# Kernel optimization log

Measured on AMD Instinct MI355X. Metric: run time of the kernel, lower is better.

## Reference

```python
import jax, jax.numpy as jnp
import numpy as np

D_IN = 1024
D_OUT = 1024
SEQ = 4096


def setup_inputs() -> dict:
    key = jax.random.key(0)
    kx, kq, kk, kv = jax.random.split(key, 4)
    x = jax.random.normal(kx, (SEQ, D_IN), dtype=jnp.float32)
    # original uses torch.rand (uniform [0,1)) for parameter init
    w_query = jax.random.uniform(kq, (D_IN, D_OUT), dtype=jnp.float32)
    w_key = jax.random.uniform(kk, (D_IN, D_OUT), dtype=jnp.float32)
    w_value = jax.random.uniform(kv, (D_IN, D_OUT), dtype=jnp.float32)
    return {"x": x, "w_query": w_query, "w_key": w_key, "w_value": w_value}


def reference(x, w_query, w_key, w_value):
    # QKV projections: [S, d_in] @ [d_in, d_out] -> [S, d_out]
    queries = x @ w_query
    keys = x @ w_key
    values = x @ w_value
    scale = keys.shape[-1] ** 0.5
    # full attention matrix [S, S]
    attn_scores = jnp.einsum('sd,td->st', queries, keys)
    attn_weights = jax.nn.softmax(attn_scores / scale, axis=-1)
    context_vecs = attn_weights @ values  # [S, d_out]
    return context_vecs
```

## Files before the change

### kernel.cpp

```cpp
#include <hip/hip_runtime.h>
#include <hip/hip_fp16.h>
#include <math.h>

#define SEQ    4096
#define DMODEL 1024

typedef _Float16 half8   __attribute__((ext_vector_type(8)));
typedef _Float16 half4v  __attribute__((ext_vector_type(4)));
typedef float    floatx4 __attribute__((ext_vector_type(4)));

__device__ inline void split_val(float v, _Float16& h, _Float16& l) {
    _Float16 hh = (_Float16)v;
    h = hh;
    l = (_Float16)(v - (float)hh);
}

__global__ __launch_bounds__(256) void prep(const float* __restrict__ x,
                                            const float* __restrict__ wq,
                                            const float* __restrict__ wk,
                                            const float* __restrict__ wv,
                                            _Float16* __restrict__ x_hi,
                                            _Float16* __restrict__ x_lo,
                                            _Float16* __restrict__ wqkT_hi,
                                            _Float16* __restrict__ wqkT_lo,
                                            _Float16* __restrict__ wvT) {
    __shared__ float tile[32][33];
    const int b = blockIdx.x;
    if (b < 3072) {
        const int which = b >> 10;
        const int bb = b & 1023;
        const int c0 = (bb & 31) * 32;
        const int r0 = (bb >> 5) * 32;
        const float* w = (which == 0) ? wq : (which == 1) ? wk : wv;
        const int tx = threadIdx.x & 31, ty = threadIdx.x >> 5;
#pragma unroll
        for (int j = 0; j < 4; ++j)
            tile[ty * 4 + j][tx] = w[(size_t)(r0 + ty * 4 + j) * DMODEL + c0 + tx];
        __syncthreads();
        if (which < 2) {
            _Float16* th = wqkT_hi + (size_t)which * DMODEL * DMODEL;
            _Float16* tl = wqkT_lo + (size_t)which * DMODEL * DMODEL;
#pragma unroll
            for (int j = 0; j < 4; ++j) {
                float v = tile[tx][ty * 4 + j];
                size_t idx = (size_t)(c0 + ty * 4 + j) * DMODEL + r0 + tx;
                _Float16 h, l;
                split_val(v, h, l);
                th[idx] = h;
                tl[idx] = l;
            }
        } else {
#pragma unroll
            for (int j = 0; j < 4; ++j)
                wvT[(size_t)(c0 + ty * 4 + j) * DMODEL + r0 + tx] =
                    (_Float16)tile[tx][ty * 4 + j];
        }
    } else {
        const int t0 = (b - 3072) * 256 + threadIdx.x;
#pragma unroll
        for (int rep = 0; rep < 4; ++rep) {
            const size_t i = (size_t)t0 + (size_t)rep * 262144;
            floatx4 v = *(const floatx4*)(x + 4 * i);
            half4v h, l;
#pragma unroll
            for (int j = 0; j < 4; ++j) {
                _Float16 hh = (_Float16)v[j];
                _Float16 ll = (_Float16)(v[j] - (float)hh);
                h[j] = hh;
                l[j] = ll;
            }
            *(half4v*)(x_hi + 4 * i) = h;
            *(half4v*)(x_lo + 4 * i) = l;
        }
    }
}

__global__ __launch_bounds__(512, 1) void gemm_qkproj_dp(
    const _Float16* __restrict__ Ahi, const _Float16* __restrict__ Alo,
    const _Float16* __restrict__ Bhi, const _Float16* __restrict__ Blo,
    _Float16* __restrict__ Qcat, _Float16* __restrict__ Kcat) {
    __shared__ _Float16 As[4][128][32];
    __shared__ _Float16 Bs[4][256][32];

    const int tid  = threadIdx.x;
    const int lane = tid & 63;
    const int wid  = tid >> 6;
    const int wm   = (wid >> 2) * 64;
    const int wn   = (wid & 3) * 64;

    const int lin = blockIdx.y * 8 + blockIdx.x;
    const int swz = (lin & 7) * 32 + (lin >> 3);
    const int rowA0 = (swz >> 3) * 128;
    const int colB0 = (swz & 7) * 256;

    const int ar  = tid >> 2;
    const int ag  = tid & 3;
    const int ags = ag ^ ((ar >> 1) & 3);
    const char* aHiB = (const char*)(Ahi + (size_t)(rowA0 + ar) * DMODEL) + ags * 16;
    const char* aLoB = (const char*)(Alo + (size_t)(rowA0 + ar) * DMODEL) + ags * 16;
    const int br  = tid >> 2;
    const int bg  = tid & 3;
    const int bgs = bg ^ ((br >> 1) & 3);
    const char* bHi0 = (const char*)(Bhi + (size_t)(colB0 + br) * DMODEL) + bgs * 16;
    const char* bHi1 = (const char*)(Bhi + (size_t)(colB0 + br + 128) * DMODEL) + bgs * 16;
    const char* bLo0 = (const char*)(Blo + (size_t)(colB0 + br) * DMODEL) + bgs * 16;
    const char* bLo1 = (const char*)(Blo + (size_t)(colB0 + br + 128) * DMODEL) + bgs * 16;

#define STAGE_QA(tt)                                                                 \
    do {                                                                             \
        const int _s = (tt) & 3;                                                     \
        const char* _ab = ((tt) < 64) ? aHiB : aLoB;                                 \
        const size_t _ko = (size_t)((tt) & 31) * 64;                                 \
        __builtin_amdgcn_global_load_lds(                                            \
            (const __attribute__((address_space(1))) void*)(_ab + _ko),              \
            (__attribute__((address_space(3))) void*)&As[_s][ar][ag * 8], 16, 0, 0); \
    } while (0)

#define STAGE_QB(tt)                                                                 \
    do {                                                                             \
        const int _s = (tt) & 3;                                                     \
        const bool _lo = ((tt) >= 32) && ((tt) < 64);                                \
        const char* _b0 = _lo ? bLo0 : bHi0;                                         \
        const char* _b1 = _lo ? bLo1 : bHi1;                                         \
        const size_t _ko = (size_t)((tt) & 31) * 64;                                 \
        __builtin_amdgcn_global_load_lds(                                            \
            (const __attribute__((address_space(1))) void*)(_b0 + _ko),              \
            (__attribute__((address_space(3))) void*)&Bs[_s][br][bg * 8], 16, 0, 0); \
        __builtin_amdgcn_global_load_lds(                                            \
            (const __attribute__((address_space(1))) void*)(_b1 + _ko),              \
            (__attribute__((address_space(3))) void*)&Bs[_s][br + 128][bg * 8], 16, 0, 0);\
    } while (0)

    const int fm = lane & 15;
    const int fq = lane >> 4;
    const int ck = (fq ^ ((fm >> 1) & 3)) * 8;

    floatx4 acc[4][4] = {};

    auto tile_body = [&](int t, bool do_stage) {
        const int s = t & 3;
        half8 av[4], bv01[2];
#pragma unroll
        for (int i = 0; i < 4; ++i) av[i] = *(const half8*)&As[s][wm + i * 16 + fm][ck];
#pragma unroll
        for (int j = 0; j < 2; ++j) bv01[j] = *(const half8*)&Bs[s][wn + j * 16 + fm][ck];
        if (do_stage) STAGE_QA(t + 3);
        asm volatile("" ::: "memory");
        __builtin_amdgcn_s_barrier();
        asm volatile("" ::: "memory");
        __builtin_amdgcn_s_setprio(1);
#pragma unroll
        for (int i = 0; i < 4; ++i)
#pragma unroll
            for (int j = 0; j < 2; ++j)
                acc[i][j] = __builtin_amdgcn_mfma_f32_16x16x32_f16(av[i], bv01[j], acc[i][j], 0, 0, 0);
        __builtin_amdgcn_s_setprio(0);
        asm volatile("" ::: "memory");
        __builtin_amdgcn_s_barrier();
        asm volatile("" ::: "memory");
        half8 bv23[2];
#pragma unroll
        for (int j = 0; j < 2; ++j) bv23[j] = *(const half8*)&Bs[s][wn + 32 + j * 16 + fm][ck];
        if (do_stage) STAGE_QB(t + 3);
        asm volatile("" ::: "memory");
        __builtin_amdgcn_s_barrier();
        asm volatile("" ::: "memory");
        __builtin_amdgcn_s_setprio(1);
#pragma unroll
        for (int i = 0; i < 4; ++i)
#pragma unroll
            for (int j = 0; j < 2; ++j)
                acc[i][j + 2] = __builtin_amdgcn_mfma_f32_16x16x32_f16(av[i], bv23[j], acc[i][j + 2], 0, 0, 0);
        __builtin_amdgcn_s_setprio(0);
    };

    STAGE_QA(0); STAGE_QB(0);
    STAGE_QA(1); STAGE_QB(1);
    STAGE_QA(2); STAGE_QB(2);
    asm volatile("s_waitcnt vmcnt(6)" ::: "memory");
    __builtin_amdgcn_s_barrier();
    asm volatile("" ::: "memory");

#pragma unroll 1
    for (int t = 0; t < 93; ++t) {
        tile_body(t, true);
        asm volatile("s_waitcnt vmcnt(6)" ::: "memory");
        __builtin_amdgcn_s_barrier();
        asm volatile("" ::: "memory");
    }
    tile_body(93, false);
    asm volatile("s_waitcnt vmcnt(3)" ::: "memory");
    __builtin_amdgcn_s_barrier();
    asm volatile("" ::: "memory");
    tile_body(94, false);
    asm volatile("s_waitcnt vmcnt(0)" ::: "memory");
    __builtin_amdgcn_s_barrier();
    asm volatile("" ::: "memory");
    tile_body(95, false);
#undef STAGE_QA
#undef STAGE_QB

    _Float16* dcat = Qcat;
    int cbase = colB0;
    if (colB0 >= 1024) { dcat = Kcat; cbase = colB0 - 1024; }

#pragma unroll
    for (int i = 0; i < 4; ++i) {
        const int growb = rowA0 + wm + i * 16 + fq * 4;
#pragma unroll
        for (int j = 0; j < 4; ++j) {
            const int gcol = wn + j * 16 + fm;
#pragma unroll
            for (int r = 0; r < 4; ++r) {
                float v = acc[i][j][r];
                size_t idx = (size_t)(growb + r) * 2048 + cbase + gcol;
                _Float16 h, l;
                split_val(v, h, l);
                dcat[idx] = h;
                dcat[idx + 1024] = l;
            }
        }
    }
}

__global__ __launch_bounds__(512, 2) void gemm_score_dp(
    const _Float16* __restrict__ Qc,
    const _Float16* __restrict__ Kc,
    _Float16* __restrict__ Ph, float* __restrict__ Marr, float* __restrict__ Larr,
    float scale) {
    __shared__ _Float16 As[4][256][32];
    __shared__ _Float16 Bs[4][256][32];

    const int tid  = threadIdx.x;
    const int lane = tid & 63;
    const int wid  = tid >> 6;
    const int wm   = (wid >> 2) * 128;
    const int wn   = (wid & 3) * 64;

    const int lin = blockIdx.y * 16 + blockIdx.x;
    const int swz = (lin & 7) * 32 + (lin >> 3);
    const int rowA0 = (swz >> 4) * 256;
    const int colB0 = (swz & 15) * 256;

    const int pr  = tid >> 2;
    const int pg  = tid & 3;
    const int pgs = pg ^ ((pr >> 1) & 3);

    const char* aSrc0 = (const char*)(Qc + (size_t)(rowA0 + pr) * 2048) + pgs * 16;
    const char* aSrc1 = (const char*)(Qc + (size_t)(rowA0 + pr + 128) * 2048) + pgs * 16;
    const char* bSrc0 = (const char*)(Kc + (size_t)(colB0 + pr) * 2048) + pgs * 16;
    const char* bSrc1 = (const char*)(Kc + (size_t)(colB0 + pr + 128) * 2048) + pgs * 16;

#define STAGE_A(t)                                                                  \
    do {                                                                            \
        const int _s = (t) & 3;                                                     \
        const size_t _ko = (size_t)(t) * 64;                                        \
        __builtin_amdgcn_global_load_lds(                                           \
            (const __attribute__((address_space(1))) void*)(aSrc0 + _ko),           \
            (__attribute__((address_space(3))) void*)&As[_s][pr][pg * 8], 16, 0, 0);\
        __builtin_amdgcn_global_load_lds(                                           \
            (const __attribute__((address_space(1))) void*)(aSrc1 + _ko),           \
            (__attribute__((address_space(3))) void*)&As[_s][pr + 128][pg * 8], 16, 0, 0);\
    } while (0)

#define STAGE_B(t)                                                                  \
    do {                                                                            \
        const int _s = (t) & 3;                                                     \
        const size_t _ko = (size_t)(t) * 64;                                        \
        __builtin_amdgcn_global_load_lds(                                           \
            (const __attribute__((address_space(1))) void*)(bSrc0 + _ko),           \
            (__attribute__((address_space(3))) void*)&Bs[_s][pr][pg * 8], 16, 0, 0);\
        __builtin_amdgcn_global_load_lds(                                           \
            (const __attribute__((address_space(1))) void*)(bSrc1 + _ko),           \
            (__attribute__((address_space(3))) void*)&Bs[_s][pr + 128][pg * 8], 16, 0, 0);\
    } while (0)

    const int fm = lane & 15;
    const int fq = lane >> 4;
    const int ck = (fq ^ ((fm >> 1) & 3)) * 8;

    floatx4 acc[8][4] = {};

    auto tile_body = [&](int t, bool do_stage) {
        const int s = t & 3;
        half8 av[4], bv[4];
#pragma unroll
        for (int i = 0; i < 4; ++i) av[i] = *(const half8*)&As[s][wm + i * 16 + fm][ck];
#pragma unroll
        for (int j = 0; j < 4; ++j) bv[j] = *(const half8*)&Bs[s][wn + j * 16 + fm][ck];
        if (do_stage) STAGE_A(t + 3);
        asm volatile("" ::: "memory");
        __builtin_amdgcn_s_barrier();
        asm volatile("" ::: "memory");
        __builtin_amdgcn_s_setprio(1);
#pragma unroll
        for (int i = 0; i < 4; ++i)
#pragma unroll
            for (int j = 0; j < 4; ++j)
                acc[i][j] = __builtin_amdgcn_mfma_f32_16x16x32_f16(av[i], bv[j], acc[i][j], 0, 0, 0);
        __builtin_amdgcn_s_setprio(0);
        asm volatile("" ::: "memory");
        __builtin_amdgcn_s_barrier();
        asm volatile("" ::: "memory");
        half8 av2[4];
#pragma unroll
        for (int i = 0; i < 4; ++i) av2[i] = *(const half8*)&As[s][wm + 64 + i * 16 + fm][ck];
        if (do_stage) STAGE_B(t + 3);
        asm volatile("" ::: "memory");
        __builtin_amdgcn_s_barrier();
        asm volatile("" ::: "memory");
        __builtin_amdgcn_s_setprio(1);
#pragma unroll
        for (int i = 0; i < 4; ++i)
#pragma unroll
            for (int j = 0; j < 4; ++j)
                acc[i + 4][j] = __builtin_amdgcn_mfma_f32_16x16x32_f16(av2[i], bv[j], acc[i + 4][j], 0, 0, 0);
        __builtin_amdgcn_s_setprio(0);
    };

    STAGE_A(0); STAGE_B(0);
    STAGE_A(1); STAGE_B(1);
    STAGE_A(2); STAGE_B(2);
    asm volatile("s_waitcnt vmcnt(8)" ::: "memory");
    __builtin_amdgcn_s_barrier();
    asm volatile("" ::: "memory");

#pragma unroll 1
    for (int t = 0; t < 61; ++t) {
        tile_body(t, true);
        asm volatile("s_waitcnt vmcnt(8)" ::: "memory");
        __builtin_amdgcn_s_barrier();
        asm volatile("" ::: "memory");
    }
    tile_body(61, false);
    asm volatile("s_waitcnt vmcnt(4)" ::: "memory");
    __builtin_amdgcn_s_barrier();
    asm volatile("" ::: "memory");
    tile_body(62, false);
    asm volatile("s_waitcnt vmcnt(0)" ::: "memory");
    __builtin_amdgcn_s_barrier();
    asm volatile("" ::: "memory");
    tile_body(63, false);
#undef STAGE_A
#undef STAGE_B

    const int tprime = (colB0 + wn) >> 6;
#pragma unroll
    for (int i = 0; i < 8; ++i) {
#pragma unroll
        for (int r = 0; r < 4; ++r) {
            const int grow = rowA0 + wm + i * 16 + fq * 4 + r;
            float s0 = acc[i][0][r] * scale;
            float s1 = acc[i][1][r] * scale;
            float s2 = acc[i][2][r] * scale;
            float s3 = acc[i][3][r] * scale;
            float mx = fmaxf(fmaxf(s0, s1), fmaxf(s2, s3));
            mx = fmaxf(mx, __shfl_xor(mx, 1));
            mx = fmaxf(mx, __shfl_xor(mx, 2));
            mx = fmaxf(mx, __shfl_xor(mx, 4));
            mx = fmaxf(mx, __shfl_xor(mx, 8));
            float p0 = __expf(s0 - mx);
            float p1 = __expf(s1 - mx);
            float p2 = __expf(s2 - mx);
            float p3 = __expf(s3 - mx);
            float sum = p0 + p1 + p2 + p3;
            sum += __shfl_xor(sum, 1);
            sum += __shfl_xor(sum, 2);
            sum += __shfl_xor(sum, 4);
            sum += __shfl_xor(sum, 8);
            _Float16* prow = Ph + (size_t)grow * SEQ + colB0 + wn + fm;
            prow[0]  = (_Float16)p0;
            prow[16] = (_Float16)p1;
            prow[32] = (_Float16)p2;
            prow[48] = (_Float16)p3;
            if (fm == 0) {
                Marr[(size_t)grow * 64 + tprime] = mx;
                Larr[(size_t)grow * 64 + tprime] = sum;
            }
        }
    }
}

__global__ __launch_bounds__(256) void reduce_scale(const float* __restrict__ Marr,
                                                    const float* __restrict__ Larr,
                                                    _Float16* __restrict__ P) {
    __shared__ float c_tab[64];
    const int tid = threadIdx.x;
    const int row = blockIdx.x;

    if (tid < 64) {
        float mt = Marr[(size_t)row * 64 + tid];
        float lt = Larr[(size_t)row * 64 + tid];
        float m = mt;
#pragma unroll
        for (int off = 32; off > 0; off >>= 1) m = fmaxf(m, __shfl_xor(m, off));
        float contrib = lt * __expf(mt - m);
        float L = contrib;
#pragma unroll
        for (int off = 32; off > 0; off >>= 1) L += __shfl_xor(L, off);
        c_tab[tid] = __expf(mt - m) / L;
    }
    __syncthreads();

    _Float16* prow = P + (size_t)row * SEQ;
#pragma unroll
    for (int i = 0; i < 4; ++i) {
        const int col = i * 1024 + (tid << 2);
        const _Float16 c = (_Float16)c_tab[col >> 6];
        half4v v = *(const half4v*)(prow + col);
        v[0] *= c; v[1] *= c; v[2] *= c; v[3] *= c;
        *(half4v*)(prow + col) = v;
    }
}

__global__ __launch_bounds__(512, 1) void gemm_pv_dp(
    const _Float16* __restrict__ P,
    const _Float16* __restrict__ VT,
    float* __restrict__ out) {
    __shared__ _Float16 As[4][128][64];
    __shared__ _Float16 Bs[4][128][64];

    const int tid  = threadIdx.x;
    const int lane = tid & 63;
    const int wid  = tid >> 6;
    const int wm   = (wid >> 2) * 64;
    const int wn   = (wid & 3) * 32;

    const int lin = blockIdx.y * 8 + blockIdx.x;
    const int swz = (lin & 7) * 32 + (lin >> 3);
    const int rowA0 = (swz >> 3) * 128;
    const int colB0 = (swz & 7) * 128;

    const int prow = tid >> 3;
    const int pgr  = tid & 7;
    const int ags  = pgr ^ (prow & 7);
    const char* aSrc0 = (const char*)(P  + (size_t)(rowA0 + prow) * SEQ) + ags * 16;
    const char* aSrc1 = (const char*)(P  + (size_t)(rowA0 + prow + 64) * SEQ) + ags * 16;
    const char* bSrc0 = (const char*)(VT + (size_t)(colB0 + prow) * SEQ) + ags * 16;
    const char* bSrc1 = (const char*)(VT + (size_t)(colB0 + prow + 64) * SEQ) + ags * 16;

#define STAGE_PA(tt)                                                                \
    do {                                                                            \
        const int _s = (tt) & 3;                                                    \
        const size_t _ko = (size_t)(tt) * 128;                                      \
        __builtin_amdgcn_global_load_lds(                                           \
            (const __attribute__((address_space(1))) void*)(aSrc0 + _ko),           \
            (__attribute__((address_space(3))) void*)&As[_s][prow][pgr * 8], 16, 0, 0);\
        __builtin_amdgcn_global_load_lds(                                           \
            (const __attribute__((address_space(1))) void*)(aSrc1 + _ko),           \
            (__attribute__((address_space(3))) void*)&As[_s][prow + 64][pgr * 8], 16, 0, 0);\
    } while (0)

#define STAGE_PB(tt)                                                                \
    do {                                                                            \
        const int _s = (tt) & 3;                                                    \
        const size_t _ko = (size_t)(tt) * 128;                                      \
        __builtin_amdgcn_global_load_lds(                                           \
            (const __attribute__((address_space(1))) void*)(bSrc0 + _ko),           \
            (__attribute__((address_space(3))) void*)&Bs[_s][prow][pgr * 8], 16, 0, 0);\
        __builtin_amdgcn_global_load_lds(                                           \
            (const __attribute__((address_space(1))) void*)(bSrc1 + _ko),           \
            (__attribute__((address_space(3))) void*)&Bs[_s][prow + 64][pgr * 8], 16, 0, 0);\
    } while (0)

    const int fm = lane & 15;
    const int fq = lane >> 4;
    const int ck0 = ((fq    ) ^ (fm & 7)) * 8;
    const int ck1 = ((fq + 4) ^ (fm & 7)) * 8;

    floatx4 acc[4][2] = {};

    auto tile_body = [&](int t, bool do_stage) {
        const int s = t & 3;
        half8 av[4], bv[2];
#pragma unroll
        for (int i = 0; i < 4; ++i) av[i] = *(const half8*)&As[s][wm + i * 16 + fm][ck0];
#pragma unroll
        for (int j = 0; j < 2; ++j) bv[j] = *(const half8*)&Bs[s][wn + j * 16 + fm][ck0];
        if (do_stage) STAGE_PA(t + 3);
        asm volatile("" ::: "memory");
        __builtin_amdgcn_s_barrier();
        asm volatile("" ::: "memory");
        __builtin_amdgcn_s_setprio(1);
#pragma unroll
        for (int i = 0; i < 4; ++i)
#pragma unroll
            for (int j = 0; j < 2; ++j)
                acc[i][j] = __builtin_amdgcn_mfma_f32_16x16x32_f16(av[i], bv[j], acc[i][j], 0, 0, 0);
        __builtin_amdgcn_s_setprio(0);
        asm volatile("" ::: "memory");
        __builtin_amdgcn_s_barrier();
        asm volatile("" ::: "memory");
        half8 av2[4], bv2[2];
#pragma unroll
        for (int i = 0; i < 4; ++i) av2[i] = *(const half8*)&As[s][wm + i * 16 + fm][ck1];
#pragma unroll
        for (int j = 0; j < 2; ++j) bv2[j] = *(const half8*)&Bs[s][wn + j * 16 + fm][ck1];
        if (do_stage) STAGE_PB(t + 3);
        asm volatile("" ::: "memory");
        __builtin_amdgcn_s_barrier();
        asm volatile("" ::: "memory");
        __builtin_amdgcn_s_setprio(1);
#pragma unroll
        for (int i = 0; i < 4; ++i)
#pragma unroll
            for (int j = 0; j < 2; ++j)
                acc[i][j] = __builtin_amdgcn_mfma_f32_16x16x32_f16(av2[i], bv2[j], acc[i][j], 0, 0, 0);
        __builtin_amdgcn_s_setprio(0);
    };

    STAGE_PA(0); STAGE_PB(0);
    STAGE_PA(1); STAGE_PB(1);
    STAGE_PA(2); STAGE_PB(2);
    asm volatile("s_waitcnt vmcnt(8)" ::: "memory");
    __builtin_amdgcn_s_barrier();
    asm volatile("" ::: "memory");

#pragma unroll 1
    for (int t = 0; t < 61; ++t) {
        tile_body(t, true);
        asm volatile("s_waitcnt vmcnt(8)" ::: "memory");
        __builtin_amdgcn_s_barrier();
        asm volatile("" ::: "memory");
    }
    tile_body(61, false);
    asm volatile("s_waitcnt vmcnt(4)" ::: "memory");
    __builtin_amdgcn_s_barrier();
    asm volatile("" ::: "memory");
    tile_body(62, false);
    asm volatile("s_waitcnt vmcnt(0)" ::: "memory");
    __builtin_amdgcn_s_barrier();
    asm volatile("" ::: "memory");
    tile_body(63, false);
#undef STAGE_PA
#undef STAGE_PB

#pragma unroll
    for (int i = 0; i < 4; ++i) {
        const int growb = rowA0 + wm + i * 16 + fq * 4;
#pragma unroll
        for (int j = 0; j < 2; ++j) {
            const int gcol = colB0 + wn + j * 16 + fm;
#pragma unroll
            for (int r = 0; r < 4; ++r)
                out[(size_t)(growb + r) * DMODEL + gcol] = acc[i][j][r];
        }
    }
}

template <int OUT_HALF>
__global__ __launch_bounds__(256) void gemm_h16_n64(
    const _Float16* __restrict__ A, int lda,
    const _Float16* __restrict__ B, int ldb,
    float* __restrict__ Cf, _Float16* __restrict__ Ch,
    int N, int K) {
    __shared__ _Float16 Ah[128][32];
    __shared__ _Float16 Bh[64][32];

    const int tid = threadIdx.x;
    const int lane = tid & 63;
    const int w = tid >> 6;
    const int wm = (w >> 1) * 64;
    const int wn = (w & 1) * 32;

    const int rowA0 = blockIdx.y * 128;
    const int colB0 = blockIdx.x * 64;

    const int sr = lane >> 2;
    const int sc = lane & 3;
    const int ra0 = w * 32 + sr;
    const int ra1 = ra0 + 16;
    const int rb0 = w * 16 + sr;
    const int cga0 = sc ^ ((ra0 >> 1) & 3);
    const int cga1 = sc ^ ((ra1 >> 1) & 3);
    const int cgb0 = sc ^ ((rb0 >> 1) & 3);

    const char* gp[3];
    gp[0] = (const char*)(A + (size_t)(rowA0 + ra0) * lda) + cga0 * 16;
    gp[1] = (const char*)(A + (size_t)(rowA0 + ra1) * lda) + cga1 * 16;
    gp[2] = (const char*)(B + (size_t)(colB0 + rb0) * ldb) + cgb0 * 16;

    _Float16* lp[3] = {
        &Ah[w * 32][0], &Ah[w * 32 + 16][0],
        &Bh[w * 16][0],
    };

    const int fm = lane & 15;
    const int fq = lane >> 4;
    const int ck = ((fq ^ ((fm >> 1) & 3)) * 8);

    floatx4 acc[4][2] = {};

    for (int k0 = 0; k0 < K; k0 += 32) {
#pragma unroll
        for (int t = 0; t < 3; ++t)
            __builtin_amdgcn_global_load_lds(
                (const __attribute__((address_space(1))) void*)gp[t],
                (__attribute__((address_space(3))) void*)lp[t], 16, 0, 0);
#pragma unroll
        for (int t = 0; t < 3; ++t) gp[t] += 64;
        __syncthreads();

        half8 av[4], bv[2];
#pragma unroll
        for (int i = 0; i < 4; ++i)
            av[i] = *(const half8*)&Ah[wm + i * 16 + fm][ck];
#pragma unroll
        for (int j = 0; j < 2; ++j)
            bv[j] = *(const half8*)&Bh[wn + j * 16 + fm][ck];
#pragma unroll
        for (int i = 0; i < 4; ++i)
#pragma unroll
            for (int j = 0; j < 2; ++j)
                acc[i][j] = __builtin_amdgcn_mfma_f32_16x16x32_f16(av[i], bv[j], acc[i][j], 0, 0, 0);
        __syncthreads();
    }

#pragma unroll
    for (int i = 0; i < 4; ++i) {
        const int growb = rowA0 + wm + i * 16 + fq * 4;
#pragma unroll
        for (int j = 0; j < 2; ++j) {
            const int gcol = colB0 + wn + j * 16 + fm;
#pragma unroll
            for (int r = 0; r < 4; ++r) {
                float v = acc[i][j][r];
                size_t idx = (size_t)(growb + r) * N + gcol;
                if (OUT_HALF) Ch[idx] = (_Float16)v;
                else          Cf[idx] = v;
            }
        }
    }
}

extern "C" void kernel_launch(void* const* d_in, const int* in_sizes, int n_in,
                              void* d_out, int out_size, void* d_ws, size_t ws_size,
                              hipStream_t stream) {
    const float* x  = (const float*)d_in[0];
    const float* wq = (const float*)d_in[1];
    const float* wk = (const float*)d_in[2];
    const float* wv = (const float*)d_in[3];
    float* out = (float*)d_out;

    char* base = (char*)d_ws;
    const size_t MB = 1u << 20;
    _Float16* P       = (_Float16*)base;
    _Float16* x_hi    = (_Float16*)(base + 0 * MB);
    _Float16* x_lo    = (_Float16*)(base + 8 * MB);
    _Float16* wqkT_hi = (_Float16*)(base + 16 * MB);
    _Float16* wqkT_lo = (_Float16*)(base + 20 * MB);
    _Float16* wvT     = (_Float16*)(base + 24 * MB);
    float*    Marr    = (float*)(base + 32 * MB);
    float*    Larr    = (float*)(base + 33 * MB);
    _Float16* Qcat    = (_Float16*)(base + 64 * MB);
    _Float16* Kcat    = (_Float16*)(base + 80 * MB);
    _Float16* VT      = (_Float16*)(base + 96 * MB);

    prep<<<4096, 256, 0, stream>>>(x, wq, wk, wv, x_hi, x_lo, wqkT_hi, wqkT_lo, wvT);

    dim3 gqk(2048 / 256, SEQ / 128);
    gemm_qkproj_dp<<<gqk, dim3(512), 0, stream>>>(x_hi, x_lo, wqkT_hi, wqkT_lo,
                                                  Qcat, Kcat);
    dim3 gvt(SEQ / 64, DMODEL / 128);
    gemm_h16_n64<1><<<gvt, 256, 0, stream>>>(wvT, DMODEL, x_hi, DMODEL,
                                             nullptr, VT, SEQ, DMODEL);

    dim3 gs(SEQ / 256, SEQ / 256);
    gemm_score_dp<<<gs, dim3(512), 0, stream>>>(Qcat, Kcat, P, Marr, Larr,
                                                1.0f / 32.0f);

    reduce_scale<<<SEQ, 256, 0, stream>>>(Marr, Larr, P);

    dim3 gpv(DMODEL / 128, SEQ / 128);
    gemm_pv_dp<<<gpv, dim3(512), 0, stream>>>(P, VT, out);
}
```

Before: 303.2 us.

## Fuse softmax rescale into PV GEMM and merge split-phase MFMA loops

The separate pass that rescaled the whole P matrix in place is replaced by a small kernel that computes per-row, per-tile scale factors into a transposed array. The PV GEMM loads these factors into shared memory and multiplies the A fragments by them before the MFMAs, removing a full read-modify-write of P. The QK projection and PV GEMMs also drop their two-phase barrier/stage split, now issuing all loads and MFMAs in one phase per tile. The swizzled block-index mapping is removed in favour of plain row-major blocks, which may change L2 locality. Scaling happens in fp16 inside the inner loop, adding VALU work and register pressure.

```diff
diff --git a/kernel.cpp b/kernel.cpp
--- a/kernel.cpp
+++ b/kernel.cpp
@@ -88,10 +88,8 @@
     const int wm   = (wid >> 2) * 64;
     const int wn   = (wid & 3) * 64;
 
-    const int lin = blockIdx.y * 8 + blockIdx.x;
-    const int swz = (lin & 7) * 32 + (lin >> 3);
-    const int rowA0 = (swz >> 3) * 128;
-    const int colB0 = (swz & 7) * 256;
+    const int rowA0 = blockIdx.y * 128;
+    const int colB0 = blockIdx.x * 256;
 
     const int ar  = tid >> 2;
     const int ag  = tid & 3;
@@ -139,12 +137,12 @@
 
     auto tile_body = [&](int t, bool do_stage) {
         const int s = t & 3;
-        half8 av[4], bv01[2];
+        half8 av[4], bv[4];
 #pragma unroll
         for (int i = 0; i < 4; ++i) av[i] = *(const half8*)&As[s][wm + i * 16 + fm][ck];
 #pragma unroll
-        for (int j = 0; j < 2; ++j) bv01[j] = *(const half8*)&Bs[s][wn + j * 16 + fm][ck];
-        if (do_stage) STAGE_QA(t + 3);
+        for (int j = 0; j < 4; ++j) bv[j] = *(const half8*)&Bs[s][wn + j * 16 + fm][ck];
+        if (do_stage) { STAGE_QA(t + 3); STAGE_QB(t + 3); }
         asm volatile("" ::: "memory");
         __builtin_amdgcn_s_barrier();
         asm volatile("" ::: "memory");
@@ -152,25 +150,8 @@
 #pragma unroll
         for (int i = 0; i < 4; ++i)
 #pragma unroll
-            for (int j = 0; j < 2; ++j)
-                acc[i][j] = __builtin_amdgcn_mfma_f32_16x16x32_f16(av[i], bv01[j], acc[i][j], 0, 0, 0);
-        __builtin_amdgcn_s_setprio(0);
-        asm volatile("" ::: "memory");
-        __builtin_amdgcn_s_barrier();
-        asm volatile("" ::: "memory");
-        half8 bv23[2];
-#pragma unroll
-        for (int j = 0; j < 2; ++j) bv23[j] = *(const half8*)&Bs[s][wn + 32 + j * 16 + fm][ck];
-        if (do_stage) STAGE_QB(t + 3);
-        asm volatile("" ::: "memory");
-        __builtin_amdgcn_s_barrier();
-        asm volatile("" ::: "memory");
-        __builtin_amdgcn_s_setprio(1);
-#pragma unroll
-        for (int i = 0; i < 4; ++i)
-#pragma unroll
-            for (int j = 0; j < 2; ++j)
-                acc[i][j + 2] = __builtin_amdgcn_mfma_f32_16x16x32_f16(av[i], bv23[j], acc[i][j + 2], 0, 0, 0);
+            for (int j = 0; j < 4; ++j)
+                acc[i][j] = __builtin_amdgcn_mfma_f32_16x16x32_f16(av[i], bv[j], acc[i][j], 0, 0, 0);
         __builtin_amdgcn_s_setprio(0);
     };
 
@@ -381,44 +362,31 @@
     }
 }
 
-__global__ __launch_bounds__(256) void reduce_scale(const float* __restrict__ Marr,
-                                                    const float* __restrict__ Larr,
-                                                    _Float16* __restrict__ P) {
-    __shared__ float c_tab[64];
-    const int tid = threadIdx.x;
+__global__ __launch_bounds__(64) void compute_c(const float* __restrict__ Marr,
+                                                const float* __restrict__ Larr,
+                                                _Float16* __restrict__ CarrT) {
     const int row = blockIdx.x;
-
-    if (tid < 64) {
-        float mt = Marr[(size_t)row * 64 + tid];
-        float lt = Larr[(size_t)row * 64 + tid];
-        float m = mt;
-#pragma unroll
-        for (int off = 32; off > 0; off >>= 1) m = fmaxf(m, __shfl_xor(m, off));
-        float contrib = lt * __expf(mt - m);
-        float L = contrib;
-#pragma unroll
-        for (int off = 32; off > 0; off >>= 1) L += __shfl_xor(L, off);
-        c_tab[tid] = __expf(mt - m) / L;
-    }
-    __syncthreads();
-
-    _Float16* prow = P + (size_t)row * SEQ;
-#pragma unroll
-    for (int i = 0; i < 4; ++i) {
-        const int col = i * 1024 + (tid << 2);
-        const _Float16 c = (_Float16)c_tab[col >> 6];
-        half4v v = *(const half4v*)(prow + col);
-        v[0] *= c; v[1] *= c; v[2] *= c; v[3] *= c;
-        *(half4v*)(prow + col) = v;
-    }
+    const int t = threadIdx.x;
+    float mt = Marr[(size_t)row * 64 + t];
+    float lt = Larr[(size_t)row * 64 + t];
+    float m = mt;
+#pragma unroll
+    for (int off = 32; off > 0; off >>= 1) m = fmaxf(m, __shfl_xor(m, off));
+    float e = __expf(mt - m);
+    float L = lt * e;
+#pragma unroll
+    for (int off = 32; off > 0; off >>= 1) L += __shfl_xor(L, off);
+    CarrT[(size_t)t * SEQ + row] = (_Float16)(e / L);
 }
 
 __global__ __launch_bounds__(512, 1) void gemm_pv_dp(
     const _Float16* __restrict__ P,
     const _Float16* __restrict__ VT,
+    const _Float16* __restrict__ CarrT,
     float* __restrict__ out) {
     __shared__ _Float16 As[4][128][64];
     __shared__ _Float16 Bs[4][128][64];
+    __shared__ _Float16 cT[64][128];
 
     const int tid  = threadIdx.x;
     const int lane = tid & 63;
@@ -426,10 +394,20 @@
     const int wm   = (wid >> 2) * 64;
     const int wn   = (wid & 3) * 32;
 
-    const int lin = blockIdx.y * 8 + blockIdx.x;
-    const int swz = (lin & 7) * 32 + (lin >> 3);
-    const int rowA0 = (swz >> 3) * 128;
-    const int colB0 = (swz & 7) * 128;
+    const int rowA0 = blockIdx.y * 128;
+    const int colB0 = blockIdx.x * 128;
+
+    {
+        int g = tid;
+#pragma unroll
+        for (int it = 0; it < 2; ++it, g += 512) {
+            const int t  = g >> 4;
+            const int r8 = (g & 15) * 8;
+            *(half8*)&cT[t][r8] =
+                *(const half8*)(CarrT + (size_t)t * SEQ + rowA0 + r8);
+        }
+    }
+    __syncthreads();
 
     const int prow = tid >> 3;
     const int pgr  = tid & 7;
@@ -472,12 +450,27 @@
 
     auto tile_body = [&](int t, bool do_stage) {
         const int s = t & 3;
-        half8 av[4], bv[2];
-#pragma unroll
-        for (int i = 0; i < 4; ++i) av[i] = *(const half8*)&As[s][wm + i * 16 + fm][ck0];
-#pragma unroll
-        for (int j = 0; j < 2; ++j) bv[j] = *(const half8*)&Bs[s][wn + j * 16 + fm][ck0];
-        if (do_stage) STAGE_PA(t + 3);
+        half8 av[4], av2[4], bv[2], bv2[2];
+        _Float16 cs[4];
+#pragma unroll
+        for (int i = 0; i < 4; ++i) {
+            av[i]  = *(const half8*)&As[s][wm + i * 16 + fm][ck0];
+            av2[i] = *(const half8*)&As[s][wm + i * 16 + fm][ck1];
+            cs[i]  = cT[t][wm + i * 16 + fm];
+        }
+#pragma unroll
+        for (int j = 0; j < 2; ++j) {
+            bv[j]  = *(const half8*)&Bs[s][wn + j * 16 + fm][ck0];
+            bv2[j] = *(const half8*)&Bs[s][wn + j * 16 + fm][ck1];
+        }
+#pragma unroll
+        for (int i = 0; i < 4; ++i)
+#pragma unroll
+            for (int e = 0; e < 8; ++e) {
+                av[i][e]  *= cs[i];
+                av2[i][e] *= cs[i];
+            }
+        if (do_stage) { STAGE_PA(t + 3); STAGE_PB(t + 3); }
         asm volatile("" ::: "memory");
         __builtin_amdgcn_s_barrier();
         asm volatile("" ::: "memory");
@@ -487,20 +480,6 @@
 #pragma unroll
             for (int j = 0; j < 2; ++j)
                 acc[i][j] = __builtin_amdgcn_mfma_f32_16x16x32_f16(av[i], bv[j], acc[i][j], 0, 0, 0);
-        __builtin_amdgcn_s_setprio(0);
-        asm volatile("" ::: "memory");
-        __builtin_amdgcn_s_barrier();
-        asm volatile("" ::: "memory");
-        half8 av2[4], bv2[2];
-#pragma unroll
-        for (int i = 0; i < 4; ++i) av2[i] = *(const half8*)&As[s][wm + i * 16 + fm][ck1];
-#pragma unroll
-        for (int j = 0; j < 2; ++j) bv2[j] = *(const half8*)&Bs[s][wn + j * 16 + fm][ck1];
-        if (do_stage) STAGE_PB(t + 3);
-        asm volatile("" ::: "memory");
-        __builtin_amdgcn_s_barrier();
-        asm volatile("" ::: "memory");
-        __builtin_amdgcn_s_setprio(1);
 #pragma unroll
         for (int i = 0; i < 4; ++i)
 #pragma unroll
@@ -652,6 +631,7 @@
     _Float16* wvT     = (_Float16*)(base + 24 * MB);
     float*    Marr    = (float*)(base + 32 * MB);
     float*    Larr    = (float*)(base + 33 * MB);
+    _Float16* CarrT   = (_Float16*)(base + 34 * MB);
     _Float16* Qcat    = (_Float16*)(base + 64 * MB);
     _Float16* Kcat    = (_Float16*)(base + 80 * MB);
     _Float16* VT      = (_Float16*)(base + 96 * MB);
@@ -669,8 +649,8 @@
     gemm_score_dp<<<gs, dim3(512), 0, stream>>>(Qcat, Kcat, P, Marr, Larr,
                                                 1.0f / 32.0f);
 
-    reduce_scale<<<SEQ, 256, 0, stream>>>(Marr, Larr, P);
+    compute_c<<<SEQ, 64, 0, stream>>>(Marr, Larr, CarrT);
 
     dim3 gpv(DMODEL / 128, SEQ / 128);
-    gemm_pv_dp<<<gpv, dim3(512), 0, stream>>>(P, VT, out);
-}
+    gemm_pv_dp<<<gpv, dim3(512), 0, stream>>>(P, VT, CarrT, out);
+}
```

Result: faster. 295.9 us (-2.4%).
